# Kernel tuning notes

Measured on AMD Instinct MI355X. Metric: run time of the kernel, lower is better.

Reference implementation:

```python
import jax, jax.numpy as jnp
import numpy as np
from jax import lax

FS = 48000.0
PI = 3.14159265358979323846

def bilinear_low_shelf(fc, gain_db, Q, fs):
    A = 10.0 ** (gain_db / 40.0)
    w0 = 2.0 * PI * fc / fs
    alpha = jnp.sin(w0) / (2.0 * Q)
    cosw = jnp.cos(w0)
    sqA = jnp.sqrt(A)
    b0 = A * (A + 1 - (A - 1) * cosw + 2 * sqA * alpha)
    b1 = 2 * A * (A - 1 - (A + 1) * cosw)
    b2 = A * (A + 1 - (A - 1) * cosw - 2 * sqA * alpha)
    a0 = A + 1 + (A - 1) * cosw + 2 * sqA * alpha
    a1 = -2 * (A - 1 + (A + 1) * cosw)
    a2 = A + 1 + (A - 1) * cosw - 2 * sqA * alpha
    return (b0 / a0, b1 / a0, b2 / a0, a1 / a0, a2 / a0)

def biquad(x, b0, b1, b2, a1, a2):
    # x: [B, T]; direct-form-II-transposed biquad with zero initial state
    B = x.shape[0]
    z0 = (jnp.zeros((B,), x.dtype), jnp.zeros((B,), x.dtype))
    def step(carry, xn):
        z1, z2 = carry
        yn = b0 * xn + z1
        z1n = b1 * xn - a1 * yn + z2
        z2n = b2 * xn - a2 * yn
        return (z1n, z2n), yn
    _, yT = lax.scan(step, z0, x.T)  # scan over time axis
    return yT.T

def setup_inputs() -> dict:
    key = jax.random.key(0)
    x = jax.random.normal(key, (64, 480000), dtype=jnp.float32)
    return {
        "x": x,
        "low_gain_db": jnp.float32(6.0),
        "mid_gain_db": jnp.float32(-3.0),
        "mid_fc": jnp.float32(800.0),
        "mid_Q": jnp.float32(1.0),
        "high_gain_db": jnp.float32(4.0),
    }

def reference(x, low_gain_db, mid_gain_db, mid_fc, mid_Q, high_gain_db):
    c = bilinear_low_shelf(jnp.float32(120.0), low_gain_db, jnp.float32(0.707), FS)
    y = biquad(x, *c)
    c = bilinear_low_shelf(mid_fc, mid_gain_db, mid_Q, FS)
    y = biquad(y, *c)
    c = bilinear_low_shelf(jnp.float32(4000.0), high_gain_db, jnp.float32(0.707), FS)
    y = biquad(y, *c)
    return y
```

## Files before the change

kernel.cpp:

```cpp
#include <hip/hip_runtime.h>
#include <math.h>


constexpr int T_LEN  = 480000;
constexpr int B_ROWS = 64;
constexpr int CHUNK  = 64;
constexpr int LOG2C  = 6;
constexpr int KCH    = T_LEN / CHUNK;
constexpr int NT     = 256;
constexpr int HISTC  = 24;
constexpr int MTERM  = 24;
constexpr int OUTC   = NT - HISTC;
constexpr int BLKROW = (KCH + OUTC - 1) / OUTC;
constexpr int NBLK   = B_ROWS * BLKROW;
constexpr int NWAVE  = NT / 64;

struct Coeffs { float b0, b1, b2, a1, a2; };

__device__ __forceinline__ float rfl(float v) {
    return __int_as_float(__builtin_amdgcn_readfirstlane(__float_as_int(v)));
}

__device__ __forceinline__ Coeffs shelf(float fc, float gdb, float Q) {
    float A  = powf(10.0f, gdb * (1.0f / 40.0f));
    float w0 = 2.0f * 3.14159265358979323846f * fc / 48000.0f;
    float sw = sinf(w0), cw = cosf(w0);
    float alpha = sw / (2.0f * Q);
    float sqA = sqrtf(A);
    float b0 = A * ((A + 1.0f) - (A - 1.0f) * cw + 2.0f * sqA * alpha);
    float b1 = 2.0f * A * ((A - 1.0f) - (A + 1.0f) * cw);
    float b2 = A * ((A + 1.0f) - (A - 1.0f) * cw - 2.0f * sqA * alpha);
    float a0 = (A + 1.0f) + (A - 1.0f) * cw + 2.0f * sqA * alpha;
    float a1 = -2.0f * ((A - 1.0f) + (A + 1.0f) * cw);
    float a2 = (A + 1.0f) + (A - 1.0f) * cw - 2.0f * sqA * alpha;
    float rr = 1.0f / a0;
    Coeffs c;
    c.b0 = rfl(b0 * rr); c.b1 = rfl(b1 * rr); c.b2 = rfl(b2 * rr);
    c.a1 = rfl(a1 * rr); c.a2 = rfl(a2 * rr);
    return c;
}

__device__ __forceinline__ float bq(float xn, const Coeffs& c, float& z1, float& z2) {
    float y = fmaf(c.b0, xn, z1);
    z1 = fmaf(-c.a1, y, fmaf(c.b1, xn, z2));
    z2 = fmaf(c.b2, xn, -(c.a2 * y));
    return y;
}

__device__ __forceinline__ float step6(float s[6], float x,
                                       const Coeffs& c1, const Coeffs& c2, const Coeffs& c3) {
    float y1 = bq(x,  c1, s[0], s[1]);
    float y2 = bq(y1, c2, s[2], s[3]);
    float y3 = bq(y2, c3, s[4], s[5]);
    return y3;
}

__global__ __launch_bounds__(256, 4) void k_fused(
    const float* __restrict__ x,
    const float* __restrict__ p_lg, const float* __restrict__ p_mg,
    const float* __restrict__ p_mf, const float* __restrict__ p_mq,
    const float* __restrict__ p_hg,
    float* __restrict__ out)
{
    __shared__ __align__(16) float smem[4096];
    __shared__ float M[36];

    const int t = threadIdx.x;
    const int r = blockIdx.x / BLKROW;
    const int b = blockIdx.x - r * BLKROW;
    const int c = b * OUTC + t - HISTC;
    const bool active = (c >= 0) && (c < KCH);

    Coeffs c1 = shelf(120.0f,  *p_lg, 0.707f);
    Coeffs c2 = shelf(*p_mf,   *p_mg, *p_mq);
    Coeffs c3 = shelf(4000.0f, *p_hg, 0.707f);

    float4 xv[16];
    {
        int cc = c < 0 ? 0 : c;
        const float4* lp = (const float4*)(x + (long long)r * T_LEN + (long long)cc * CHUNK);
        if (active) {
            #pragma unroll
            for (int q = 0; q < 16; ++q) xv[q] = lp[q];
        } else {
            #pragma unroll
            for (int q = 0; q < 16; ++q) xv[q] = make_float4(0.f, 0.f, 0.f, 0.f);
        }
    }

    float s[6] = {0.f, 0.f, 0.f, 0.f, 0.f, 0.f};
    #pragma unroll
    for (int q = 0; q < 16; ++q) {
        step6(s, xv[q].x, c1, c2, c3);
        step6(s, xv[q].y, c1, c2, c3);
        step6(s, xv[q].z, c1, c2, c3);
        step6(s, xv[q].w, c1, c2, c3);
    }
    #pragma unroll
    for (int i = 0; i < 6; ++i) smem[t * 7 + i] = s[i];

    if (t < 6) {
        float e[6] = {0.f, 0.f, 0.f, 0.f, 0.f, 0.f};
        e[t] = 1.0f;
        step6(e, 0.0f, c1, c2, c3);
        #pragma unroll
        for (int i = 0; i < 6; ++i) M[i * 6 + t] = e[i];
    }
    __syncthreads();
    for (int it = 0; it < LOG2C; ++it) {
        float acc = 0.f;
        if (t < 36) {
            int i = t / 6, j = t - 6 * (t / 6);
            #pragma unroll
            for (int q = 0; q < 6; ++q) acc = fmaf(M[i * 6 + q], M[q * 6 + j], acc);
        }
        __syncthreads();
        if (t < 36) M[t] = acc;
        __syncthreads();
    }
    float a[36];
    #pragma unroll
    for (int i = 0; i < 36; ++i) a[i] = rfl(M[i]);

    float t6[6] = {0.f, 0.f, 0.f, 0.f, 0.f, 0.f};
    int m0 = t - MTERM; if (m0 < 0) m0 = 0;
    for (int m = m0; m < t; ++m) {
        float dm[6];
        #pragma unroll
        for (int i = 0; i < 6; ++i) dm[i] = smem[m * 7 + i];
        float nt6[6];
        #pragma unroll
        for (int i = 0; i < 6; ++i) {
            float acc = dm[i];
            #pragma unroll
            for (int j = 0; j < 6; ++j) acc = fmaf(a[i * 6 + j], t6[j], acc);
            nt6[i] = acc;
        }
        #pragma unroll
        for (int i = 0; i < 6; ++i) t6[i] = nt6[i];
    }

    #pragma unroll
    for (int q = 0; q < 16; ++q) {
        float4 v = xv[q];
        v.x = step6(t6, v.x, c1, c2, c3);
        v.y = step6(t6, v.y, c1, c2, c3);
        v.z = step6(t6, v.z, c1, c2, c3);
        v.w = step6(t6, v.w, c1, c2, c3);
        xv[q] = v;
    }

    __syncthreads();
    float4* sv = (float4*)smem;
    const int slot = t & 63;
    const int wv   = t >> 6;
    float4* op = (float4*)(out + (long long)r * T_LEN);
    for (int rr = 0; rr < NWAVE; ++rr) {
        if (wv == rr) {
            #pragma unroll
            for (int q = 0; q < 16; ++q) {
                int byte = (slot * 256 + q * 16) ^ ((slot & 7) << 4);
                sv[byte >> 4] = xv[q];
            }
        }
        __syncthreads();
        const int chunkBase = b * OUTC + 64 * rr - HISTC;
        #pragma unroll
        for (int j = 0; j < 4; ++j) {
            int f  = 256 * j + t;
            int aa = f >> 4;
            int qq = f & 15;
            int tr = 64 * rr + aa;
            int cc = chunkBase + aa;
            if (tr >= HISTC && cc < KCH) {
                int byte = (aa * 256 + qq * 16) ^ ((aa & 7) << 4);
                op[(long long)cc * 16 + qq] = sv[byte >> 4];
            }
        }
        __syncthreads();
    }
}

extern "C" void kernel_launch(void* const* d_in, const int* in_sizes, int n_in,
                              void* d_out, int out_size, void* d_ws, size_t ws_size,
                              hipStream_t stream) {
    const float* x  = (const float*)d_in[0];
    const float* lg = (const float*)d_in[1];
    const float* mg = (const float*)d_in[2];
    const float* mf = (const float*)d_in[3];
    const float* mq = (const float*)d_in[4];
    const float* hg = (const float*)d_in[5];
    float* out = (float*)d_out;

    hipLaunchKernelGGL(k_fused, dim3(NBLK), dim3(NT), 0, stream,
                       x, lg, mg, mf, mq, hg, out);
}
```

Baseline: 242.0 us.

## Replace second biquad pass with precomputed impulse-response correction from carry state

The first pass now keeps the zero-state outputs. The second serial 64-step triple-biquad pass is replaced by adding a linear correction: each output gets a dot product of the incoming 6-element state with a precomputed per-position response table held in shared memory. This removes the second dependent recurrence chain. It adds shared-memory loads and a serial table build by six threads. The history length is cut from 24 to 21 chunks and the launch-bounds occupancy hint is raised from 4 to 8, which may force register pressure or spills and slightly changes numerical truncation.

```diff
diff --git a/kernel.cpp b/kernel.cpp
--- a/kernel.cpp
+++ b/kernel.cpp
@@ -8,8 +8,8 @@
 constexpr int LOG2C  = 6;
 constexpr int KCH    = T_LEN / CHUNK;
 constexpr int NT     = 256;
-constexpr int HISTC  = 24;
-constexpr int MTERM  = 24;
+constexpr int HISTC  = 21;
+constexpr int MTERM  = 21;
 constexpr int OUTC   = NT - HISTC;
 constexpr int BLKROW = (KCH + OUTC - 1) / OUTC;
 constexpr int NBLK   = B_ROWS * BLKROW;
@@ -55,7 +55,19 @@
     return y3;
 }
 
-__global__ __launch_bounds__(256, 4) void k_fused(
+__device__ __forceinline__ float corr(float y0, const float* cnp, const float t6[6]) {
+    float4 ca = *(const float4*)(cnp);
+    float2 cb = *(const float2*)(cnp + 4);
+    float acc = fmaf(ca.x, t6[0], y0);
+    acc = fmaf(ca.y, t6[1], acc);
+    acc = fmaf(ca.z, t6[2], acc);
+    acc = fmaf(ca.w, t6[3], acc);
+    acc = fmaf(cb.x, t6[4], acc);
+    acc = fmaf(cb.y, t6[5], acc);
+    return acc;
+}
+
+__global__ __launch_bounds__(256, 8) void k_fused(
     const float* __restrict__ x,
     const float* __restrict__ p_lg, const float* __restrict__ p_mg,
     const float* __restrict__ p_mf, const float* __restrict__ p_mq,
@@ -64,6 +76,7 @@
 {
     __shared__ __align__(16) float smem[4096];
     __shared__ float M[36];
+    __shared__ __align__(16) float cn[64 * 8];
 
     const int t = threadIdx.x;
     const int r = blockIdx.x / BLKROW;
@@ -91,10 +104,12 @@
     float s[6] = {0.f, 0.f, 0.f, 0.f, 0.f, 0.f};
     #pragma unroll
     for (int q = 0; q < 16; ++q) {
-        step6(s, xv[q].x, c1, c2, c3);
-        step6(s, xv[q].y, c1, c2, c3);
-        step6(s, xv[q].z, c1, c2, c3);
-        step6(s, xv[q].w, c1, c2, c3);
+        float4 v = xv[q];
+        v.x = step6(s, v.x, c1, c2, c3);
+        v.y = step6(s, v.y, c1, c2, c3);
+        v.z = step6(s, v.z, c1, c2, c3);
+        v.w = step6(s, v.w, c1, c2, c3);
+        xv[q] = v;
     }
     #pragma unroll
     for (int i = 0; i < 6; ++i) smem[t * 7 + i] = s[i];
@@ -122,6 +137,16 @@
     #pragma unroll
     for (int i = 0; i < 36; ++i) a[i] = rfl(M[i]);
 
+    if ((t >> 6) == 1 && (t & 63) < 6) {
+        const int j = t & 63;
+        float e[6];
+        #pragma unroll
+        for (int i = 0; i < 6; ++i) e[i] = (i == j) ? 1.0f : 0.0f;
+        for (int n = 0; n < 64; ++n) {
+            cn[n * 8 + j] = step6(e, 0.0f, c1, c2, c3);
+        }
+    }
+
     float t6[6] = {0.f, 0.f, 0.f, 0.f, 0.f, 0.f};
     int m0 = t - MTERM; if (m0 < 0) m0 = 0;
     for (int m = m0; m < t; ++m) {
@@ -140,17 +165,18 @@
         for (int i = 0; i < 6; ++i) t6[i] = nt6[i];
     }
 
+    __syncthreads();
+
     #pragma unroll
     for (int q = 0; q < 16; ++q) {
         float4 v = xv[q];
-        v.x = step6(t6, v.x, c1, c2, c3);
-        v.y = step6(t6, v.y, c1, c2, c3);
-        v.z = step6(t6, v.z, c1, c2, c3);
-        v.w = step6(t6, v.w, c1, c2, c3);
+        v.x = corr(v.x, cn + (4 * q + 0) * 8, t6);
+        v.y = corr(v.y, cn + (4 * q + 1) * 8, t6);
+        v.z = corr(v.z, cn + (4 * q + 2) * 8, t6);
+        v.w = corr(v.w, cn + (4 * q + 3) * 8, t6);
         xv[q] = v;
     }
 
-    __syncthreads();
     float4* sv = (float4*)smem;
     const int slot = t & 63;
     const int wv   = t >> 6;
```

Result: slower. 305.0 us (+26.0%).
